# Kernel tuning notes

Measured on AMD Instinct MI355X. Metric: run time of the kernel, lower is better.

Reference implementation:

```python
import jax, jax.numpy as jnp
import numpy as np

B, N_BOX, AH, AW = 16, 2048, 256, 256

def setup_inputs() -> dict:
    key = jax.random.key(0)
    k1, k2, k3, k4, k5 = jax.random.split(key, 5)
    # logits in [0,1): matches the original code path where attention_map[attention_map>=0]
    # keeps every element (so BCE runs over the full map)
    attention_mask = jax.random.uniform(k1, (B, 1, AH, AW), dtype=jnp.float32)
    # YOLO-style targets [n,6] = (batch_id, class, xc, yc, w, h) normalized, sorted by batch_id
    bidx = jnp.sort(jax.random.randint(k2, (N_BOX,), 0, B)).astype(jnp.float32)
    cls = jax.random.randint(k3, (N_BOX,), 0, 80).astype(jnp.float32)
    xy = jax.random.uniform(k4, (N_BOX, 2), minval=0.05, maxval=0.95)
    wh = jax.random.uniform(k5, (N_BOX, 2), minval=0.01, maxval=0.25)
    target = jnp.concatenate([bidx[:, None], cls[:, None], xy, wh], axis=1).astype(jnp.float32)
    return {"attention_mask": attention_mask, "target": target,
            "batch_size": B, "img_h": 1024, "img_w": 1024}

def _loss(attention_mask, target, batch_size, img_h, img_w):
    ah, aw = attention_mask.shape[2], attention_mask.shape[3]
    bidx = target[:, 0].astype(jnp.int32)                      # [n]
    xc, yc, bw, bh = target[:, 2], target[:, 3], target[:, 4], target[:, 5]
    # xywhn2xyxy (padw=padh=0)
    x1 = img_w * (xc - bw / 2)
    y1 = img_h * (yc - bh / 2)
    x2 = img_w * (xc + bw / 2)
    y2 = img_h * (yc + bh / 2)
    valid = (x1 <= img_w) & (y1 <= img_h) & (x2 <= img_w) & (y2 <= img_h)
    # scale to attention-map resolution
    sx, sy = aw / img_w, ah / img_h
    X1 = jnp.clip(jnp.trunc(x1 * sx), 0).astype(jnp.int32)     # int() truncation then max(.,0)
    Y1 = jnp.clip(jnp.trunc(y1 * sy), 0).astype(jnp.int32)
    X2 = jnp.minimum(jnp.ceil(x2 * sx) + 1, aw).astype(jnp.int32)
    Y2 = jnp.minimum(jnp.ceil(y2 * sy) + 1, ah).astype(jnp.int32)
    ys = jnp.arange(ah)
    xs = jnp.arange(aw)
    in_y = (ys[None, :] >= Y1[:, None]) & (ys[None, :] < Y2[:, None])   # [n,ah]
    in_x = (xs[None, :] >= X1[:, None]) & (xs[None, :] < X2[:, None])   # [n,aw]
    rect = (in_y[:, :, None] & in_x[:, None, :]) & valid[:, None, None]  # [n,ah,aw]
    # OR of per-box rectangles per image (scatter-rasterize)
    cover = jax.ops.segment_sum(rect.astype(jnp.float32), bidx, num_segments=batch_size)
    mask_gt = (cover > 0).astype(jnp.float32)                  # [B,ah,aw]
    has_box = jax.ops.segment_sum(jnp.ones_like(bidx), bidx, num_segments=batch_size) > 0
    logits = attention_mask[:, 0]                              # [B,ah,aw]
    # BCEWithLogitsLoss (mean reduction), numerically stable
    bce = jnp.maximum(logits, 0) - logits * mask_gt + jnp.log1p(jnp.exp(-jnp.abs(logits)))
    per_batch = bce.mean(axis=(1, 2))
    # images with no annotation are skipped (try/except continue)
    return jnp.sum(jnp.where(has_box, per_batch, 0.0))

def reference(attention_mask, target, batch_size, img_h, img_w):
    return _loss(attention_mask, target, batch_size, img_h, img_w)
```

## Files before the change

### kernel.cpp

```cpp
#include <hip/hip_runtime.h>

#define B_SZ 16
#define N_BOX 2048
#define AH 256
#define AW 256
#define ROWS 8

__global__ __launch_bounds__(256) void prep_kernel(
    const float* __restrict__ target,
    const int*   __restrict__ img_h_p,
    const int*   __restrict__ img_w_p,
    int4*        __restrict__ rects,
    int*         __restrict__ starts,
    float*       __restrict__ out)
{
    int i = blockIdx.x * blockDim.x + threadIdx.x;
    if (i == 0) out[0] = 0.0f;
    if (i >= N_BOX) return;

    float fh = (float)img_h_p[0];
    float fw = (float)img_w_p[0];

    const float* t = target + (size_t)i * 6;
    float xc = t[2], yc = t[3], bw = t[4], bh = t[5];

    float x1 = fw * (xc - bw * 0.5f);
    float y1 = fh * (yc - bh * 0.5f);
    float x2 = fw * (xc + bw * 0.5f);
    float y2 = fh * (yc + bh * 0.5f);

    bool valid = (x1 <= fw) && (y1 <= fh) && (x2 <= fw) && (y2 <= fh);

    float sx = (float)AW / fw;
    float sy = (float)AH / fh;

    int X1 = (int)fmaxf(truncf(x1 * sx), 0.0f);
    int Y1 = (int)fmaxf(truncf(y1 * sy), 0.0f);
    int X2 = (int)fminf(ceilf(x2 * sx) + 1.0f, (float)AW);
    int Y2 = (int)fminf(ceilf(y2 * sy) + 1.0f, (float)AH);

    if (!valid) { X1 = 0; X2 = 0; Y1 = 0; Y2 = 0; }
    rects[i] = make_int4(X1, Y1, X2, Y2);

    int b  = (int)t[0];
    int bp = (i == 0) ? -1 : (int)target[(size_t)(i - 1) * 6];
    for (int k = bp + 1; k <= b; ++k) starts[k] = i;
    if (i == N_BOX - 1)
        for (int k = b + 1; k <= B_SZ; ++k) starts[k] = N_BOX;
}

__global__ __launch_bounds__(256) void main_kernel(
    const float* __restrict__ mask,
    const int4*  __restrict__ rects,
    const int*   __restrict__ starts,
    float*       __restrict__ out)
{
    const int b  = blockIdx.y;
    const int y0 = blockIdx.x * ROWS;
    const int x  = threadIdx.x;

    __shared__ float s_red[4];

    const int s   = starts[b];
    const int e   = starts[b + 1];
    const int cnt = e - s;

    unsigned cov = 0;
    for (int j = s; j < e; ++j) {
        const int4 r = rects[j];
        if (r.y < y0 + ROWS && r.w > y0) {
            const int lo = max(r.y - y0, 0);
            const int hi = min(r.w - y0, ROWS);
            const unsigned rowbits = ((1u << (hi - lo)) - 1u) << lo;
            const bool xin = (x >= r.x) && (x < r.z);
            cov |= xin ? rowbits : 0u;
        }
    }

    float acc = 0.0f;
    #pragma unroll
    for (int r = 0; r < ROWS; ++r) {
        const float l = mask[((size_t)b * AH + (y0 + r)) * AW + x];
        const float m = (float)((cov >> r) & 1u);
        acc += fmaxf(l, 0.0f) - l * m + log1pf(expf(-fabsf(l)));
    }

    #pragma unroll
    for (int off = 32; off > 0; off >>= 1) acc += __shfl_down(acc, off, 64);
    const int wave = x >> 6;
    if ((x & 63) == 0) s_red[wave] = acc;
    __syncthreads();
    if (x == 0) {
        const float sum = s_red[0] + s_red[1] + s_red[2] + s_red[3];
        if (cnt > 0)
            atomicAdd(out, sum * (1.0f / (float)(AH * AW)));
    }
}

extern "C" void kernel_launch(void* const* d_in, const int* in_sizes, int n_in,
                              void* d_out, int out_size, void* d_ws, size_t ws_size,
                              hipStream_t stream) {
    const float* attention_mask = (const float*)d_in[0];
    const float* target         = (const float*)d_in[1];
    const int*   img_h          = (const int*)d_in[3];
    const int*   img_w          = (const int*)d_in[4];

    int4* rects  = (int4*)d_ws;
    int*  starts = (int*)((char*)d_ws + (size_t)N_BOX * sizeof(int4));
    float* out   = (float*)d_out;

    prep_kernel<<<(N_BOX + 255) / 256, 256, 0, stream>>>(
        target, img_h, img_w, rects, starts, out);

    dim3 grid(AH / ROWS, B_SZ);
    main_kernel<<<grid, 256, 0, stream>>>(attention_mask, rects, starts, out);
}
```

Baseline: 82.27 us.

## Fuse box prep into main kernel with per-block shared-memory rect filtering

Removes the separate prep kernel: each block scans all boxes itself, keeps those belonging to its image and overlapping its row band, and packs them into a compact 32-bit entry list in shared memory. The coverage loop then reads the short filtered list from LDS instead of every rect of the image from global memory. The output is zeroed with a memset instead of inside the prep kernel. In exchange, every block redundantly reads the whole target array and uses shared atomics to build its list.

```diff
diff --git a/kernel.cpp b/kernel.cpp
--- a/kernel.cpp
+++ b/kernel.cpp
@@ -6,75 +6,65 @@
 #define AW 256
 #define ROWS 8
 
-__global__ __launch_bounds__(256) void prep_kernel(
+__global__ __launch_bounds__(256) void fused_kernel(
     const float* __restrict__ target,
+    const float* __restrict__ mask,
     const int*   __restrict__ img_h_p,
     const int*   __restrict__ img_w_p,
-    int4*        __restrict__ rects,
-    int*         __restrict__ starts,
     float*       __restrict__ out)
 {
-    int i = blockIdx.x * blockDim.x + threadIdx.x;
-    if (i == 0) out[0] = 0.0f;
-    if (i >= N_BOX) return;
-
-    float fh = (float)img_h_p[0];
-    float fw = (float)img_w_p[0];
-
-    const float* t = target + (size_t)i * 6;
-    float xc = t[2], yc = t[3], bw = t[4], bh = t[5];
-
-    float x1 = fw * (xc - bw * 0.5f);
-    float y1 = fh * (yc - bh * 0.5f);
-    float x2 = fw * (xc + bw * 0.5f);
-    float y2 = fh * (yc + bh * 0.5f);
-
-    bool valid = (x1 <= fw) && (y1 <= fh) && (x2 <= fw) && (y2 <= fh);
-
-    float sx = (float)AW / fw;
-    float sy = (float)AH / fh;
-
-    int X1 = (int)fmaxf(truncf(x1 * sx), 0.0f);
-    int Y1 = (int)fmaxf(truncf(y1 * sy), 0.0f);
-    int X2 = (int)fminf(ceilf(x2 * sx) + 1.0f, (float)AW);
-    int Y2 = (int)fminf(ceilf(y2 * sy) + 1.0f, (float)AH);
-
-    if (!valid) { X1 = 0; X2 = 0; Y1 = 0; Y2 = 0; }
-    rects[i] = make_int4(X1, Y1, X2, Y2);
-
-    int b  = (int)t[0];
-    int bp = (i == 0) ? -1 : (int)target[(size_t)(i - 1) * 6];
-    for (int k = bp + 1; k <= b; ++k) starts[k] = i;
-    if (i == N_BOX - 1)
-        for (int k = b + 1; k <= B_SZ; ++k) starts[k] = N_BOX;
-}
-
-__global__ __launch_bounds__(256) void main_kernel(
-    const float* __restrict__ mask,
-    const int4*  __restrict__ rects,
-    const int*   __restrict__ starts,
-    float*       __restrict__ out)
-{
-    const int b  = blockIdx.y;
-    const int y0 = blockIdx.x * ROWS;
+    const int b  = blockIdx.x >> 5;
+    const int y0 = (blockIdx.x & 31) * ROWS;
     const int x  = threadIdx.x;
 
+    __shared__ unsigned s_list[N_BOX];
+    __shared__ int   s_n;
+    __shared__ int   s_has;
     __shared__ float s_red[4];
 
-    const int s   = starts[b];
-    const int e   = starts[b + 1];
-    const int cnt = e - s;
+    if (x == 0) { s_n = 0; s_has = 0; }
+    __syncthreads();
 
+    const float fh = (float)img_h_p[0];
+    const float fw = (float)img_w_p[0];
+    const float sx = (float)AW / fw;
+    const float sy = (float)AH / fh;
+
+    for (int base = 0; base < N_BOX; base += 256) {
+        const float* t = target + (size_t)(base + x) * 6;
+        const int bi = (int)t[0];
+        if (bi == b) {
+            s_has = 1;
+            const float xc = t[2], yc = t[3], bw = t[4], bh = t[5];
+            const float x1 = fw * (xc - bw * 0.5f);
+            const float y1 = fh * (yc - bh * 0.5f);
+            const float x2 = fw * (xc + bw * 0.5f);
+            const float y2 = fh * (yc + bh * 0.5f);
+            const bool valid = (x1 <= fw) && (y1 <= fh) &&
+                               (x2 <= fw) && (y2 <= fh);
+            const int X1 = (int)fmaxf(truncf(x1 * sx), 0.0f);
+            const int Y1 = (int)fmaxf(truncf(y1 * sy), 0.0f);
+            const int X2 = (int)fminf(ceilf(x2 * sx) + 1.0f, (float)AW);
+            const int Y2 = (int)fminf(ceilf(y2 * sy) + 1.0f, (float)AH);
+            if (valid && X1 < X2 && Y1 < y0 + ROWS && Y2 > y0) {
+                const int lo = max(Y1 - y0, 0);
+                const int hi = min(Y2 - y0, ROWS);
+                const unsigned rowbits = ((1u << (hi - lo)) - 1u) << lo;
+                const unsigned entry = (unsigned)X1 | ((unsigned)X2 << 9)
+                                     | (rowbits << 18);
+                s_list[atomicAdd(&s_n, 1)] = entry;
+            }
+        }
+    }
+    __syncthreads();
+
+    const int n = s_n;
     unsigned cov = 0;
-    for (int j = s; j < e; ++j) {
-        const int4 r = rects[j];
-        if (r.y < y0 + ROWS && r.w > y0) {
-            const int lo = max(r.y - y0, 0);
-            const int hi = min(r.w - y0, ROWS);
-            const unsigned rowbits = ((1u << (hi - lo)) - 1u) << lo;
-            const bool xin = (x >= r.x) && (x < r.z);
-            cov |= xin ? rowbits : 0u;
-        }
+    for (int j = 0; j < n; ++j) {
+        const unsigned e = s_list[j];
+        const int X1 = (int)(e & 511u);
+        const int X2 = (int)((e >> 9) & 511u);
+        cov |= (x >= X1 && x < X2) ? (e >> 18) : 0u;
     }
 
     float acc = 0.0f;
@@ -87,13 +77,11 @@
 
     #pragma unroll
     for (int off = 32; off > 0; off >>= 1) acc += __shfl_down(acc, off, 64);
-    const int wave = x >> 6;
-    if ((x & 63) == 0) s_red[wave] = acc;
+    if ((x & 63) == 0) s_red[x >> 6] = acc;
     __syncthreads();
-    if (x == 0) {
+    if (x == 0 && s_has) {
         const float sum = s_red[0] + s_red[1] + s_red[2] + s_red[3];
-        if (cnt > 0)
-            atomicAdd(out, sum * (1.0f / (float)(AH * AW)));
+        atomicAdd(out, sum * (1.0f / (float)(AH * AW)));
     }
 }
 
@@ -104,14 +92,10 @@
     const float* target         = (const float*)d_in[1];
     const int*   img_h          = (const int*)d_in[3];
     const int*   img_w          = (const int*)d_in[4];
+    float*       out            = (float*)d_out;
 
-    int4* rects  = (int4*)d_ws;
-    int*  starts = (int*)((char*)d_ws + (size_t)N_BOX * sizeof(int4));
-    float* out   = (float*)d_out;
+    hipMemsetAsync(out, 0, sizeof(float), stream);
 
-    prep_kernel<<<(N_BOX + 255) / 256, 256, 0, stream>>>(
-        target, img_h, img_w, rects, starts, out);
-
-    dim3 grid(AH / ROWS, B_SZ);
-    main_kernel<<<grid, 256, 0, stream>>>(attention_mask, rects, starts, out);
+    fused_kernel<<<B_SZ * (AH / ROWS), 256, 0, stream>>>(
+        target, attention_mask, img_h, img_w, out);
 }
```

After: 74.39 us. 1.11x faster.
